# Kernel tuning notes

Hardware: AMD Instinct MI355X
Metric: run time of the kernel (lower is better)

## Reference

```python
import jax, jax.numpy as jnp
import numpy as np

D = 512      # feature dim d
N = 8192     # context length n
LMBD = 0.9   # eligibility trace decay


def _build_consts():
    two_d1 = 2 * D + 1
    # P: single nonzero entry at bottom-right
    P = np.zeros((two_d1, two_d1), dtype=np.float32)
    P[-1, -1] = 1.0
    # M: (n+1)x(n+1); top-left n x n block is lower-triangular lmbd^(row-col),
    # last row and last column are all zero (M[-1,-1] set to 0 in torch code)
    i = np.arange(N)
    diff = i[:, None] - i[None, :]
    Mnn = np.where(diff >= 0, LMBD ** np.maximum(diff, 0), 0.0).astype(np.float32)
    M = np.zeros((N + 1, N + 1), dtype=np.float32)
    M[:N, :N] = Mnn
    # Q: top-left 2d x 2d block = [[-I, I], [0, 0]]
    I = np.eye(D, dtype=np.float32)
    Q = np.zeros((two_d1, two_d1), dtype=np.float32)
    Q[:D, :D] = -I
    Q[:D, D:2 * D] = I
    return jnp.asarray(P), jnp.asarray(M), jnp.asarray(Q)


def setup_inputs() -> dict:
    key = jax.random.key(0)
    kz, = jax.random.split(key, 1)
    Z = jax.random.normal(kz, (2 * D + 1, N + 1), dtype=jnp.float32)
    alpha = jnp.ones((1,), dtype=jnp.float32)  # learned parameter
    P, M, Q = _build_consts()
    return {"Z": Z, "alpha": alpha, "P": P, "M": M, "Q": Q}


def reference(Z, alpha, P, M, Q):
    # Z: (2d+1, n+1). Matches torch: Z + alpha/n * P @ Z @ M @ Z.T @ Q @ Z
    n = Z.shape[1] - 1
    upd = ((((P @ Z) @ M) @ Z.T) @ Q) @ Z  # left-to-right like torch's @ chain
    return Z + (alpha[0] / n) * upd
```

## Files before the change

kernel.cpp:

```cpp
#include <hip/hip_runtime.h>

#define ND   512
#define NN   8192
#define NP1  8193

typedef float f4 __attribute__((ext_vector_type(4)));

#define NWB   512
#define NCPB  512
#define CTHR  131072u
#define HI_BEG   1048704u
#define LAST_BEG 2097408u
#define F4_END   2099456u
#define TAILF    8397824u

template<int A>
__device__ __forceinline__ void scan_dot(const float* __restrict__ Z,
                                         size_t rowbase, int t,
                                         const f4* __restrict__ z4,
                                         float* __restrict__ es,
                                         float* __restrict__ red,
                                         float* __restrict__ wout) {
    constexpr int NW = (A == 0) ? 8 : 9;
    const f4* __restrict__ aw = (const f4*)(Z + rowbase - A) + 8 * t;
    f4 W[NW];
#pragma unroll
    for (int m = 0; m < NW; ++m) W[m] = aw[m];

    const float L1 = 0.9f;
    float e = W[A >> 2][A & 3];
#pragma unroll
    for (int i = 1; i < 32; ++i)
        e = fmaf(L1, e, W[(A + i) >> 2][(A + i) & 3]);
    es[t] = e;
    __syncthreads();

    const float l2 = L1 * L1, l4v = l2 * l2, l8 = l4v * l4v;
    const float l16 = l8 * l8, lam32 = l16 * l16;
    float C = 0.f;
#pragma unroll
    for (int k = 7; k >= 1; --k) {
        float ek = (t - k >= 0) ? es[t - k] : 0.f;
        C = fmaf(lam32, C, ek);
    }

    float q = C, acc = 0.f;
#pragma unroll
    for (int m = 0; m < 8; ++m) {
        f4 zz = z4[8 * t + m];
#pragma unroll
        for (int e2 = 0; e2 < 4; ++e2) {
            const int i = 4 * m + e2;
            q = fmaf(L1, q, W[(A + i) >> 2][(A + i) & 3]);
            acc = fmaf(zz[e2], q, acc);
        }
    }

    for (int off = 32; off > 0; off >>= 1)
        acc += __shfl_down(acc, off, 64);
    if ((t & 63) == 0) red[t >> 6] = acc;
    __syncthreads();
    if (t == 0) *wout = (red[0] + red[1]) + (red[2] + red[3]);
}

__global__ __launch_bounds__(256) void kMain(const float* __restrict__ Z,
                                             float* __restrict__ w,
                                             float* __restrict__ out) {
    const int b = blockIdx.x;
    const int t = threadIdx.x;

    if (b < NWB) {
        __shared__ float es[256];
        __shared__ float red[4];
        const int c = b;
        const size_t base = (size_t)c * NP1;
        const int a   = c & 3;
        const int pre = (4 - a) & 3;
        const int nq  = (NP1 - pre) >> 2;

        {
            const f4* __restrict__ src = (const f4*)(Z + base + pre);
            f4* __restrict__ dst = (f4*)(out + base + pre);
            f4 xv[8];
#pragma unroll
            for (int m = 0; m < 8; ++m) {
                int i = t + 256 * m;
                xv[m] = (i < nq) ? src[i] : (f4){0.f, 0.f, 0.f, 0.f};
            }
#pragma unroll
            for (int m = 0; m < 8; ++m) {
                int i = t + 256 * m;
                if (i < nq) __builtin_nontemporal_store(xv[m], &dst[i]);
            }
            if (t == 0) {
                for (int e = 0; e < pre; ++e)
                    __builtin_nontemporal_store(Z[base + e], &out[base + e]);
                for (int j = pre + 4 * nq; j < NP1; ++j)
                    __builtin_nontemporal_store(Z[base + j], &out[base + j]);
            }
        }

        const f4* __restrict__ z4 = (const f4*)(Z + (size_t)(2 * ND) * NP1);
        switch (a) {
            case 0: scan_dot<0>(Z, base, t, z4, es, red, &w[c]); break;
            case 1: scan_dot<1>(Z, base, t, z4, es, red, &w[c]); break;
            case 2: scan_dot<2>(Z, base, t, z4, es, red, &w[c]); break;
            default: scan_dot<3>(Z, base, t, z4, es, red, &w[c]); break;
        }
    } else {
        const f4* __restrict__ src = (const f4*)Z;
        f4* __restrict__ dst = (f4*)out;
        unsigned tid = (unsigned)(b - NWB) * 256u + (unsigned)t;
        unsigned i = HI_BEG + tid;
#pragma unroll
        for (int m = 0; m < 8; ++m) {
            f4 x = src[i];
            __builtin_nontemporal_store(x, &dst[i]);
            i += CTHR;
        }
        if (i < F4_END) {
            f4 x = src[i];
            if (i >= LAST_BEG) dst[i] = x;
            else __builtin_nontemporal_store(x, &dst[i]);
        }
        if (tid == 0u) out[TAILF] = Z[TAILF];
    }
}

__global__ __launch_bounds__(256) void kFin(const float* __restrict__ Z,
                                            const float* __restrict__ w,
                                            const float* __restrict__ alpha,
                                            float* __restrict__ out) {
    int b = blockIdx.x;
    int xcd = b & 7;
    int q   = b >> 3;
    int cyh = q / 33;
    int jx  = q - 33 * cyh;
    int cy  = cyh * 8 + xcd;
    int j = jx * 256 + threadIdx.x;
    if (j >= NP1) return;
    int c0 = cy * 16;
    const size_t DS = (size_t)ND * NP1;
    float acc0 = 0.f, acc1 = 0.f;
#pragma unroll
    for (int cb = 0; cb < 16; cb += 4) {
        int c = c0 + cb;
        size_t base = (size_t)c * NP1 + (size_t)j;
        float lo0 = Z[base          ], lo1 = Z[base +     NP1];
        float lo2 = Z[base + 2 * NP1], lo3 = Z[base + 3 * NP1];
        float hi0 = Z[base + DS          ], hi1 = Z[base + DS +     NP1];
        float hi2 = Z[base + DS + 2 * NP1], hi3 = Z[base + DS + 3 * NP1];
        acc0 = fmaf(w[c],     hi0 - lo0, acc0);
        acc1 = fmaf(w[c + 1], hi1 - lo1, acc1);
        acc0 = fmaf(w[c + 2], hi2 - lo2, acc0);
        acc1 = fmaf(w[c + 3], hi3 - lo3, acc1);
    }
    float s = alpha[0] * (1.0f / (float)NN);
    atomicAdd(&out[(size_t)(2 * ND) * NP1 + j], s * (acc0 + acc1));
}

extern "C" void kernel_launch(void* const* d_in, const int* in_sizes, int n_in,
                              void* d_out, int out_size, void* d_ws, size_t ws_size,
                              hipStream_t stream) {
    const float* Z     = (const float*)d_in[0];
    const float* alpha = (const float*)d_in[1];
    float* out = (float*)d_out;

    float* w = (float*)d_ws;

    kMain<<<NWB + NCPB, 256, 0, stream>>>(Z, w, out);
    kFin<<<1056, 256, 0, stream>>>(Z, w, alpha, out);
}
```

Baseline: 23.07 us.

## Fuse row copy into scan loads and simplify kFin grid indexing

The per-row copy of Z to out in the first 512 blocks is folded into the scan routine: the same f4 registers loaded for the eligibility-trace scan are now stored to the output, so each row is read from global memory once instead of twice. The copy uses aligned f4 windows starting at base-A, so the misaligned-edge scalar handling is replaced by an extra f4 store from the last thread. The finishing kernel drops its XCD-aware block swizzle for a plain 2D grid, which simplifies indexing but may change L2 locality across chiplets. Neighbouring rows' aligned windows overlap at their edges, so some elements are written by two blocks with identical values.

```diff
diff --git a/kernel.cpp b/kernel.cpp
--- a/kernel.cpp
+++ b/kernel.cpp
@@ -15,17 +15,30 @@
 #define TAILF    8397824u
 
 template<int A>
-__device__ __forceinline__ void scan_dot(const float* __restrict__ Z,
-                                         size_t rowbase, int t,
-                                         const f4* __restrict__ z4,
-                                         float* __restrict__ es,
-                                         float* __restrict__ red,
-                                         float* __restrict__ wout) {
+__device__ __forceinline__ void row_fused(const float* __restrict__ Z,
+                                          float* __restrict__ out,
+                                          size_t base, int t,
+                                          const f4* __restrict__ z4,
+                                          float* __restrict__ es,
+                                          float* __restrict__ red,
+                                          float* __restrict__ wout) {
     constexpr int NW = (A == 0) ? 8 : 9;
-    const f4* __restrict__ aw = (const f4*)(Z + rowbase - A) + 8 * t;
+    const f4* __restrict__ src = (const f4*)(Z + base - A);
+    f4* __restrict__ dst = (f4*)(out + base - A);
+
     f4 W[NW];
 #pragma unroll
-    for (int m = 0; m < NW; ++m) W[m] = aw[m];
+    for (int m = 0; m < NW; ++m) W[m] = src[8 * t + m];
+    f4 Tl;
+    if (A == 0 && t == 255) Tl = src[2048];
+
+#pragma unroll
+    for (int m = 0; m < 8; ++m)
+        __builtin_nontemporal_store(W[m], &dst[8 * t + m]);
+    if (t == 255) {
+        if (A == 0) __builtin_nontemporal_store(Tl, &dst[2048]);
+        else        __builtin_nontemporal_store(W[8], &dst[2048]);
+    }
 
     const float L1 = 0.9f;
     float e = W[A >> 2][A & 3];
@@ -74,38 +87,12 @@
         __shared__ float red[4];
         const int c = b;
         const size_t base = (size_t)c * NP1;
-        const int a   = c & 3;
-        const int pre = (4 - a) & 3;
-        const int nq  = (NP1 - pre) >> 2;
-
-        {
-            const f4* __restrict__ src = (const f4*)(Z + base + pre);
-            f4* __restrict__ dst = (f4*)(out + base + pre);
-            f4 xv[8];
-#pragma unroll
-            for (int m = 0; m < 8; ++m) {
-                int i = t + 256 * m;
-                xv[m] = (i < nq) ? src[i] : (f4){0.f, 0.f, 0.f, 0.f};
-            }
-#pragma unroll
-            for (int m = 0; m < 8; ++m) {
-                int i = t + 256 * m;
-                if (i < nq) __builtin_nontemporal_store(xv[m], &dst[i]);
-            }
-            if (t == 0) {
-                for (int e = 0; e < pre; ++e)
-                    __builtin_nontemporal_store(Z[base + e], &out[base + e]);
-                for (int j = pre + 4 * nq; j < NP1; ++j)
-                    __builtin_nontemporal_store(Z[base + j], &out[base + j]);
-            }
-        }
-
         const f4* __restrict__ z4 = (const f4*)(Z + (size_t)(2 * ND) * NP1);
-        switch (a) {
-            case 0: scan_dot<0>(Z, base, t, z4, es, red, &w[c]); break;
-            case 1: scan_dot<1>(Z, base, t, z4, es, red, &w[c]); break;
-            case 2: scan_dot<2>(Z, base, t, z4, es, red, &w[c]); break;
-            default: scan_dot<3>(Z, base, t, z4, es, red, &w[c]); break;
+        switch (c & 3) {
+            case 0: row_fused<0>(Z, out, base, t, z4, es, red, &w[c]); break;
+            case 1: row_fused<1>(Z, out, base, t, z4, es, red, &w[c]); break;
+            case 2: row_fused<2>(Z, out, base, t, z4, es, red, &w[c]); break;
+            default: row_fused<3>(Z, out, base, t, z4, es, red, &w[c]); break;
         }
     } else {
         const f4* __restrict__ src = (const f4*)Z;
@@ -131,15 +118,9 @@
                                             const float* __restrict__ w,
                                             const float* __restrict__ alpha,
                                             float* __restrict__ out) {
-    int b = blockIdx.x;
-    int xcd = b & 7;
-    int q   = b >> 3;
-    int cyh = q / 33;
-    int jx  = q - 33 * cyh;
-    int cy  = cyh * 8 + xcd;
-    int j = jx * 256 + threadIdx.x;
+    int j = blockIdx.x * 256 + threadIdx.x;
     if (j >= NP1) return;
-    int c0 = cy * 16;
+    int c0 = blockIdx.y * 16;
     const size_t DS = (size_t)ND * NP1;
     float acc0 = 0.f, acc1 = 0.f;
 #pragma unroll
@@ -169,5 +150,5 @@
     float* w = (float*)d_ws;
 
     kMain<<<NWB + NCPB, 256, 0, stream>>>(Z, w, out);
-    kFin<<<1056, 256, 0, stream>>>(Z, w, alpha, out);
+    kFin<<<dim3(33, 32), 256, 0, stream>>>(Z, w, alpha, out);
 }
```

New measurement: 49.98 us. 117% more time.
